# Performance work log

Measured on AMD Instinct MI355X. Metric: run time of the kernel, lower is better.

## Reference

```python
import jax, jax.numpy as jnp
import numpy as np

NH = 16   # num heads
CS = 16   # inner chunk size

def _gelu(x):
    return jax.nn.gelu(x, approximate=True)

def _diff_gelu(x):
    t = jnp.tanh(0.79788456 * x * (1.0 + 0.044715 * x * x))
    return 0.5 * x * ((1.0 - t * t) * (0.79788456 + 0.1070322243 * x * x)) + 0.5 * (1.0 + t)

def _ln_fused_l2_bwd(x, tgt, gamma, beta, eps=1e-6):
    # x, tgt: [B*nh, CS, f]; gamma/beta: [1, nh, 1, f]
    Bnh, N, HF = x.shape
    mu = x.mean(-1, keepdims=True)
    var = x.var(-1, keepdims=True)
    std = jnp.sqrt(var + eps)
    x_hat = (x - mu) / std
    y = gamma * x_hat.reshape(-1, NH, N, HF) + beta
    go = y - tgt.reshape(-1, NH, N, HF)
    gxh = (go * gamma).reshape(Bnh, N, HF)
    return (HF * gxh - gxh.sum(-1, keepdims=True) - x_hat * (gxh * x_hat).sum(-1, keepdims=True)) / (HF * std)

def setup_inputs() -> dict:
    key = jax.random.key(0)
    ks = jax.random.split(key, 8)
    B, nh, f, hf4, n_chunks = 4, NH, 64, 256, 128
    Bnh = B * nh
    XQ = jax.random.normal(ks[0], (n_chunks, Bnh, CS, f), jnp.float32)
    XK = jax.random.normal(ks[1], (n_chunks, Bnh, CS, f), jnp.float32)
    XV = jax.random.normal(ks[2], (n_chunks, Bnh, CS, f), jnp.float32)
    # inner-loop lr coeffs (ilr * token_idx ~ lr/head_dim): small positive
    coeff = jax.random.uniform(ks[3], (n_chunks, Bnh, CS, 1), jnp.float32) * 0.01
    coeff_last = jax.random.uniform(ks[4], (n_chunks, Bnh, 1, 1), jnp.float32) * 0.01
    W1 = jax.random.normal(ks[5], (Bnh, f, hf4), jnp.float32) * 0.02
    b1 = jnp.zeros((Bnh, 1, hf4), jnp.float32)
    W2 = jax.random.normal(ks[6], (Bnh, hf4, f), jnp.float32) * 0.02
    b2 = jnp.zeros((Bnh, 1, f), jnp.float32)
    ln_weight = jnp.ones((1, nh, 1, f), jnp.float32)
    ln_bias = jnp.zeros((1, nh, 1, f), jnp.float32)
    return dict(XQ=XQ, XK=XK, XV=XV, coeff=coeff, coeff_last=coeff_last,
                W1=W1, b1=b1, W2=W2, b2=b2, ln_weight=ln_weight, ln_bias=ln_bias)

def reference(XQ, XK, XV, coeff, coeff_last, W1, b1, W2, b2, ln_weight, ln_bias):
    n_chunks, Bnh, _, f = XQ.shape
    attn_b = jnp.tril(jnp.ones((CS, CS), XQ.dtype))

    def step(carry, inp):
        W1c, b1c, W2c, b2c = carry
        xv, xk, xq, c, cl = inp
        Z1 = xk @ W1c + b1c                      # [Bnh, CS, 4f]
        X2 = _gelu(Z1)
        Z2 = X2 @ W2c + b2c                      # [Bnh, CS, f]
        dZ2 = _ln_fused_l2_bwd(Z2, xv - xk, ln_weight, ln_bias)
        dZ1 = (dZ2 @ W2c.transpose(0, 2, 1)) * _diff_gelu(Z1)
        b1_bar = b1c - c * (attn_b @ dZ1)
        A1 = jnp.tril(xq @ xk.transpose(0, 2, 1))
        Z1_bar = xq @ W1c - c * (A1 @ dZ1) + b1_bar
        X2_bar = _gelu(Z1_bar)
        b2_bar = b2c - c * (attn_b @ dZ2)
        A2 = jnp.tril(X2_bar @ X2.transpose(0, 2, 1))
        Z2_bar = X2_bar @ W2c - c * (A2 @ dZ2) + b2_bar
        W1n = W1c - cl * (xk.transpose(0, 2, 1) @ dZ1)
        W2n = W2c - cl * (X2.transpose(0, 2, 1) @ dZ2)
        return (W1n, b1_bar[:, -1:], W2n, b2_bar[:, -1:]), Z2_bar

    _, Z2_all = jax.lax.scan(step, (W1, b1, W2, b2), (XV, XK, XQ, coeff, coeff_last))
    # [n_chunks, Bnh, CS, f] -> [Bnh, N, f]
    return Z2_all.transpose(1, 0, 2, 3).reshape(Bnh, n_chunks * CS, f)
```

## Files before the change

kernel.cpp:

```cpp
#include <hip/hip_runtime.h>

typedef __attribute__((ext_vector_type(8))) short bf16x8;
typedef __attribute__((ext_vector_type(4))) float f32x4;
typedef __attribute__((ext_vector_type(2))) unsigned int u32x2;

#define MFMA16(a,b,c) __builtin_amdgcn_mfma_f32_16x16x32_bf16(a,b,c,0,0,0)
#define A_GELU 0.7978845608028654f

#define OFF_W1B   0u
#define OFF_W2F   36864u
#define OFF_XK    70656u
#define OFF_XQ    72960u
#define OFF_X2    75264u
#define OFF_X2B   83712u
#define OFF_DZ2B  92160u
#define OFF_DZ1CT 94464u
#define OFF_DZ2CT 114944u
#define OFF_XKCT  120064u
#define OFF_X2CT  125184u
#define OFF_M1    145664u
#define OFF_M2    146944u
#define OFF_Z2F   148224u
#define OFF_Z2G   152576u
#define OFF_TGT   156928u
#define OFF_B2    161024u
#define OFF_COEF  161536u
#define OFF_CL    161600u
#define SMEM_BYTES 161616u

#define W2COL(col, row) ((col) ^ (((row)&7)<<3))

__device__ __forceinline__ float fast_tanh(float u){
    float e = __expf(2.0f*u);
    return 1.0f - 2.0f/(e + 1.0f);
}
__device__ __forceinline__ float gelu_f(float x){
    float t = fast_tanh(A_GELU*(x + 0.044715f*x*x*x));
    return 0.5f*x*(1.0f+t);
}
__device__ __forceinline__ float dgelu_f(float x){
    float x2 = x*x;
    float t = fast_tanh(A_GELU*x*(1.0f + 0.044715f*x2));
    return 0.5f*x*((1.0f-t*t)*(A_GELU + 0.1070322243f*x2)) + 0.5f*(1.0f+t);
}
__device__ __forceinline__ short f2bf(float f){
    unsigned u = __builtin_bit_cast(unsigned, f);
    u += 0x7FFFu + ((u >> 16) & 1u);
    return (short)(u >> 16);
}
__device__ __forceinline__ float bf2f(unsigned short s){
    unsigned u = ((unsigned)s) << 16;
    return __builtin_bit_cast(float, u);
}
__device__ __forceinline__ unsigned pkbf(float a, float b){
    unsigned r;
    asm("v_cvt_pk_bf16_f32 %0, %1, %2" : "=v"(r) : "v"(a), "v"(b));
    return r;
}
__device__ __forceinline__ bf16x8 ldfrag(const unsigned short* p){
    return *(const bf16x8*)p;
}

__global__ __launch_bounds__(512, 1)
void ttt_m2(const float* __restrict__ XQ, const float* __restrict__ XK,
            const float* __restrict__ XV, const float* __restrict__ coeff,
            const float* __restrict__ coeff_last,
            const float* __restrict__ W1g, const float* __restrict__ b1g,
            const float* __restrict__ W2g, const float* __restrict__ b2g,
            const float* __restrict__ gammag, const float* __restrict__ betag,
            float* __restrict__ out)
{
    const int h  = blockIdx.x;
    const int t  = threadIdx.x;
    const int l  = t & 63;
    const int w  = t >> 6;
    const int lo = l & 15;
    const int hi = l >> 4;

    extern __shared__ char smem[];
    unsigned short* sW1bu  = (unsigned short*)(smem + OFF_W1B);
    unsigned short* sW2fu  = (unsigned short*)(smem + OFF_W2F);
    unsigned short* sxku   = (unsigned short*)(smem + OFF_XK);
    unsigned short* sxqu   = (unsigned short*)(smem + OFF_XQ);
    unsigned short* sX2u   = (unsigned short*)(smem + OFF_X2);
    unsigned short* sX2bu  = (unsigned short*)(smem + OFF_X2B);
    unsigned short* sdZ2bu = (unsigned short*)(smem + OFF_DZ2B);
    unsigned short* sdZ1ct = (unsigned short*)(smem + OFF_DZ1CT);
    unsigned short* sdZ2ct = (unsigned short*)(smem + OFF_DZ2CT);
    unsigned short* sxkct  = (unsigned short*)(smem + OFF_XKCT);
    unsigned short* sX2ct  = (unsigned short*)(smem + OFF_X2CT);
    unsigned short* sM1u   = (unsigned short*)(smem + OFF_M1);
    unsigned short* sM2u   = (unsigned short*)(smem + OFF_M2);
    float* sZ2f  = (float*)(smem + OFF_Z2F);
    float* sZ2g  = (float*)(smem + OFF_Z2G);
    float* stgt  = (float*)(smem + OFF_TGT);
    float* b2f   = (float*)(smem + OFF_B2);
    float* scoef = (float*)(smem + OFF_COEF);
    float* sCL   = (float*)(smem + OFF_CL);

    const int base1 = h*16384;
    const int base2 = h*16384;

    float mW1[4][2][4];
    float mW2[2][4][4];
    #pragma unroll
    for (int mt = 0; mt < 4; ++mt)
      #pragma unroll
      for (int tix = 0; tix < 2; ++tix)
        #pragma unroll
        for (int reg = 0; reg < 4; ++reg) {
            const int m = mt*16 + hi*4 + reg, n = (2*w + tix)*16 + lo;
            mW1[mt][tix][reg] = W1g[base1 + m*256 + n];
        }
    #pragma unroll
    for (int mi = 0; mi < 2; ++mi)
      #pragma unroll
      for (int nt = 0; nt < 4; ++nt)
        #pragma unroll
        for (int reg = 0; reg < 4; ++reg) {
            const int m = (2*w + mi)*16 + hi*4 + reg, n = nt*16 + lo;
            mW2[mi][nt][reg] = W2g[base2 + m*64 + n];
        }
    float b1reg[2];
    b1reg[0] = b1g[h*256 + (2*w)*16 + lo];
    b1reg[1] = b1g[h*256 + (2*w+1)*16 + lo];

    for (int i = 0; i < 32; ++i) {
        const int idx = i*512 + t;
        const int m = idx >> 8, n = idx & 255;
        sW1bu[n*72 + m] = f2bf(W1g[base1 + idx]);
    }
    for (int i = 0; i < 32; ++i) {
        const int idx = i*512 + t;
        const int hf = idx >> 6, f = idx & 63;
        sW2fu[f*264 + W2COL(hf, f)] = f2bf(W2g[base2 + idx]);
    }
    if (t < 64) b2f[t] = b2g[h*64 + t];
    if (t < 256) {
        for (int k = 16; k < 40; ++k) { sdZ1ct[t*40 + k] = 0; sX2ct[t*40 + k] = 0; }
    }
    if (t < 64) {
        for (int k = 16; k < 40; ++k) { sdZ2ct[t*40 + k] = 0; sxkct[t*40 + k] = 0; }
    }
    if (t < 16) {
        for (int k = 16; k < 40; ++k) { sM1u[t*40 + k] = 0; sM2u[t*40 + k] = 0; }
    }

    const float gj = gammag[(h & 15)*64 + l];
    const float bj = betag [(h & 15)*64 + l];
    __syncthreads();

    for (int ci = 0; ci < 128; ++ci) {
        const int cb = ci*65536 + h*1024;

        {
            const int r0 = w*2;
            const float xk0 = XK[cb + r0*64 + l],     xq0 = XQ[cb + r0*64 + l];
            const float xk1 = XK[cb + (r0+1)*64 + l], xq1 = XQ[cb + (r0+1)*64 + l];
            const float xv0 = XV[cb + r0*64 + l],     xv1 = XV[cb + (r0+1)*64 + l];
            const unsigned pkk = pkbf(xk0, xk1);
            const unsigned pkq = pkbf(xq0, xq1);
            sxku[r0*72 + l]     = (unsigned short)pkk;
            sxku[(r0+1)*72 + l] = (unsigned short)(pkk >> 16);
            sxqu[r0*72 + l]     = (unsigned short)pkq;
            sxqu[(r0+1)*72 + l] = (unsigned short)(pkq >> 16);
            *(unsigned*)&sxkct[l*40 + r0] = pkk;
            stgt[r0*64 + l]     = xv0 - xk0;
            stgt[(r0+1)*64 + l] = xv1 - xk1;
        }
        if (t < 16)  scoef[t] = coeff[ci*1024 + h*16 + t];
        if (t == 16) sCL[0]   = coeff_last[ci*64 + h];
        __syncthreads();
        const float clv = sCL[0];
        const float c15 = scoef[15];

        float z1s[8];
        bf16x8 afk0 = ldfrag(sxku + lo*72 + hi*8);
        bf16x8 afk1 = ldfrag(sxku + lo*72 + 32 + hi*8);
        #pragma unroll
        for (int tix = 0; tix < 2; ++tix) {
            const int n = (2*w + tix)*16 + lo;
            f32x4 acc = {b1reg[tix], b1reg[tix], b1reg[tix], b1reg[tix]};
            acc = MFMA16(afk0, ldfrag(sW1bu + n*72 + hi*8), acc);
            acc = MFMA16(afk1, ldfrag(sW1bu + n*72 + 32 + hi*8), acc);
            float g[4];
            #pragma unroll
            for (int reg = 0; reg < 4; ++reg) {
                z1s[tix*4 + reg] = acc[reg];
                g[reg] = gelu_f(acc[reg]);
            }
            const unsigned p01 = pkbf(g[0], g[1]), p23 = pkbf(g[2], g[3]);
            sX2u[(hi*4+0)*264 + n] = (unsigned short)p01;
            sX2u[(hi*4+1)*264 + n] = (unsigned short)(p01 >> 16);
            sX2u[(hi*4+2)*264 + n] = (unsigned short)p23;
            sX2u[(hi*4+3)*264 + n] = (unsigned short)(p23 >> 16);
            *(u32x2*)&sX2ct[n*40 + hi*4] = (u32x2){p01, p23};
        }
        if (w == 0) {
            bf16x8 aq0 = ldfrag(sxqu + lo*72 + hi*8);
            bf16x8 aq1 = ldfrag(sxqu + lo*72 + 32 + hi*8);
            f32x4 a1 = {0.f, 0.f, 0.f, 0.f};
            a1 = MFMA16(aq0, afk0, a1);
            a1 = MFMA16(aq1, afk1, a1);
            #pragma unroll
            for (int reg = 0; reg < 4; ++reg) {
                const int r = hi*4 + reg;
                const float cr = scoef[r];
                const float v = (lo <= r) ? (-cr*(a1[reg] + 1.0f)) : 0.0f;
                sM1u[r*40 + lo] = f2bf(v);
            }
        }
        __syncthreads();

        const int tile = w & 3, kh = w >> 2;
        const int nf = tile*16 + lo;
        {
            f32x4 accPB;
            if (kh == 0) {
                const float b2v = b2f[(ci & 1)*64 + nf];
                accPB = (f32x4){b2v, b2v, b2v, b2v};
            } else accPB = (f32x4){0.f, 0.f, 0.f, 0.f};
            #pragma unroll
            for (int s = 0; s < 4; ++s) {
                const int k = (kh*4 + s)*32 + hi*8;
                accPB = MFMA16(ldfrag(sX2u + lo*264 + k),
                               ldfrag(sW2fu + nf*264 + W2COL(k, nf)), accPB);
            }
            float* dst = (kh == 0) ? sZ2g : sZ2f;
            #pragma unroll
            for (int reg = 0; reg < 4; ++reg)
                dst[(hi*4 + reg)*68 + nf] = accPB[reg];
        }
        __syncthreads();

        {
            float dzp[2];
            #pragma unroll
            for (int i = 0; i < 2; ++i) {
                const int r = w*2 + i;
                const float z2 = sZ2f[r*68 + l] + sZ2g[r*68 + l];
                float s1 = z2, s2 = z2*z2;
                #pragma unroll
                for (int m = 1; m < 64; m <<= 1) { s1 += __shfl_xor(s1, m); s2 += __shfl_xor(s2, m); }
                const float mu   = s1*(1.0f/64.0f);
                const float var  = s2*(1.0f/64.0f) - mu*mu;
                const float rstd = rsqrtf(var + 1e-6f);
                const float xh   = (z2 - mu)*rstd;
                const float go   = gj*xh + bj - stgt[r*64 + l];
                const float gg   = go*gj;
                float u1 = gg, u2 = gg*xh;
                #pragma unroll
                for (int m = 1; m < 64; m <<= 1) { u1 += __shfl_xor(u1, m); u2 += __shfl_xor(u2, m); }
                dzp[i] = (64.0f*gg - u1 - xh*u2)*(rstd*(1.0f/64.0f));
            }
            const unsigned pk = pkbf(dzp[0], dzp[1]);
            sdZ2bu[(w*2)*72 + l]   = (unsigned short)pk;
            sdZ2bu[(w*2+1)*72 + l] = (unsigned short)(pk >> 16);
            *(unsigned*)&sdZ2ct[l*40 + w*2] = pk;
        }
        __syncthreads();

        float b1old[2];
        {
            bf16x8 ad0 = ldfrag(sdZ2bu + lo*72 + hi*8);
            bf16x8 ad1 = ldfrag(sdZ2bu + lo*72 + 32 + hi*8);
            #pragma unroll
            for (int tix = 0; tix < 2; ++tix) {
                const int n = (2*w + tix)*16 + lo;
                f32x4 acc = {0.f, 0.f, 0.f, 0.f};
                bf16x8 bw;
                #pragma unroll
                for (int j = 0; j < 8; ++j)
                    bw[j] = (short)sW2fu[(hi*8 + j)*264 + (n ^ (j<<3))];
                acc = MFMA16(ad0, bw, acc);
                #pragma unroll
                for (int j = 0; j < 8; ++j)
                    bw[j] = (short)sW2fu[(32 + hi*8 + j)*264 + (n ^ (j<<3))];
                acc = MFMA16(ad1, bw, acc);
                float dv[4];
                float cs = 0.f;
                #pragma unroll
                for (int reg = 0; reg < 4; ++reg) {
                    dv[reg] = acc[reg]*dgelu_f(z1s[tix*4 + reg]);
                    cs += dv[reg];
                }
                *(u32x2*)&sdZ1ct[n*40 + hi*4] =
                    (u32x2){pkbf(dv[0], dv[1]), pkbf(dv[2], dv[3])};
                cs += __shfl_xor(cs, 16);
                cs += __shfl_xor(cs, 32);
                b1old[tix] = b1reg[tix];
                b1reg[tix] -= c15*cs;
            }
        }
        __syncthreads();

        {
            bf16x8 aq0 = ldfrag(sxqu + lo*72 + hi*8);
            bf16x8 aq1 = ldfrag(sxqu + lo*72 + 32 + hi*8);
            bf16x8 am1 = ldfrag(sM1u + lo*40 + hi*8);
            #pragma unroll
            for (int tix = 0; tix < 2; ++tix) {
                const int n = (2*w + tix)*16 + lo;
                f32x4 acc = {b1old[tix], b1old[tix], b1old[tix], b1old[tix]};
                acc = MFMA16(aq0, ldfrag(sW1bu + n*72 + hi*8), acc);
                acc = MFMA16(aq1, ldfrag(sW1bu + n*72 + 32 + hi*8), acc);
                acc = MFMA16(am1, ldfrag(sdZ1ct + n*40 + hi*8), acc);
                float g[4];
                #pragma unroll
                for (int reg = 0; reg < 4; ++reg) g[reg] = gelu_f(acc[reg]);
                const unsigned p01 = pkbf(g[0], g[1]), p23 = pkbf(g[2], g[3]);
                sX2bu[(hi*4+0)*264 + n] = (unsigned short)p01;
                sX2bu[(hi*4+1)*264 + n] = (unsigned short)(p01 >> 16);
                sX2bu[(hi*4+2)*264 + n] = (unsigned short)p23;
                sX2bu[(hi*4+3)*264 + n] = (unsigned short)(p23 >> 16);
            }
            bf16x8 bz0 = ldfrag(sdZ1ct + ((2*w)*16 + lo)*40 + hi*8);
            bf16x8 bz1 = ldfrag(sdZ1ct + ((2*w+1)*16 + lo)*40 + hi*8);
            #pragma unroll
            for (int mt = 0; mt < 4; ++mt) {
                bf16x8 axt = ldfrag(sxkct + (mt*16 + lo)*40 + hi*8);
                f32x4 z4 = {0.f,0.f,0.f,0.f};
                f32x4 u0 = MFMA16(axt, bz0, z4);
                f32x4 u1 = MFMA16(axt, bz1, z4);
                #pragma unroll
                for (int reg = 0; reg < 4; ++reg) {
                    mW1[mt][0][reg] -= clv*u0[reg];
                    mW1[mt][1][reg] -= clv*u1[reg];
                }
            }
        }
        __syncthreads();

        {
            bf16x8 bz2[4];
            #pragma unroll
            for (int nt = 0; nt < 4; ++nt)
                bz2[nt] = ldfrag(sdZ2ct + (nt*16 + lo)*40 + hi*8);
            #pragma unroll
            for (int mi = 0; mi < 2; ++mi) {
                bf16x8 ax2 = ldfrag(sX2ct + ((2*w + mi)*16 + lo)*40 + hi*8);
                #pragma unroll
                for (int nt = 0; nt < 4; ++nt) {
                    f32x4 z4 = {0.f,0.f,0.f,0.f};
                    f32x4 u = MFMA16(ax2, bz2[nt], z4);
                    #pragma unroll
                    for (int reg = 0; reg < 4; ++reg)
                        mW2[mi][nt][reg] -= clv*u[reg];
                }
            }
            if (w == 0) {
                f32x4 a2 = {0.f,0.f,0.f,0.f};
                #pragma unroll
                for (int ks = 0; ks < 8; ++ks) {
                    const int k = ks*32 + hi*8;
                    a2 = MFMA16(ldfrag(sX2bu + lo*264 + k),
                                ldfrag(sX2u + lo*264 + k), a2);
                }
                #pragma unroll
                for (int reg = 0; reg < 4; ++reg) {
                    const int r = hi*4 + reg;
                    const float cr = scoef[r];
                    const float v = (lo <= r) ? (-cr*(a2[reg] + 1.0f)) : 0.0f;
                    sM2u[r*40 + lo] = f2bf(v);
                }
            }
            if (w == 1) {
                float cs = 0.f;
                #pragma unroll
                for (int k = 0; k < 16; ++k) cs += bf2f(sdZ2ct[l*40 + k]);
                b2f[((ci+1) & 1)*64 + l] = b2f[(ci & 1)*64 + l] - c15*cs;
            }
        }
        __syncthreads();

        f32x4 accPF;
        if (kh == 0) {
            const float b2v = b2f[(ci & 1)*64 + nf];
            accPF = (f32x4){b2v, b2v, b2v, b2v};
        } else accPF = (f32x4){0.f, 0.f, 0.f, 0.f};
        #pragma unroll
        for (int s = 0; s < 4; ++s) {
            const int k = (kh*4 + s)*32 + hi*8;
            accPF = MFMA16(ldfrag(sX2bu + lo*264 + k),
                           ldfrag(sW2fu + nf*264 + W2COL(k, nf)), accPF);
        }
        if (kh == 0) {
            accPF = MFMA16(ldfrag(sM2u + lo*40 + hi*8),
                           ldfrag(sdZ2ct + nf*40 + hi*8), accPF);
        } else {
            #pragma unroll
            for (int reg = 0; reg < 4; ++reg)
                sZ2f[(hi*4 + reg)*68 + nf] = accPF[reg];
        }
        __syncthreads();

        if (kh == 0) {
            #pragma unroll
            for (int reg = 0; reg < 4; ++reg) {
                const int r = hi*4 + reg;
                out[h*131072 + (ci*16 + r)*64 + nf] = accPF[reg] + sZ2f[r*68 + nf];
            }
        }
        #pragma unroll
        for (int mt = 0; mt < 4; ++mt)
          #pragma unroll
          for (int tix = 0; tix < 2; ++tix) {
                const int n = (2*w + tix)*16 + lo, m0 = mt*16 + hi*4;
                *(u32x2*)&sW1bu[n*72 + m0] =
                    (u32x2){pkbf(mW1[mt][tix][0], mW1[mt][tix][1]),
                            pkbf(mW1[mt][tix][2], mW1[mt][tix][3])};
          }
        #pragma unroll
        for (int mi = 0; mi < 2; ++mi)
          #pragma unroll
          for (int nt = 0; nt < 4; ++nt) {
                const int n = nt*16 + lo, m0 = (2*w + mi)*16 + hi*4;
                *(u32x2*)&sW2fu[n*264 + (m0 ^ ((n&7)<<3))] =
                    (u32x2){pkbf(mW2[mi][nt][0], mW2[mi][nt][1]),
                            pkbf(mW2[mi][nt][2], mW2[mi][nt][3])};
          }
        __syncthreads();
    }
}

extern "C" void kernel_launch(void* const* d_in, const int* in_sizes, int n_in,
                              void* d_out, int out_size, void* d_ws, size_t ws_size,
                              hipStream_t stream) {
    const float* XQ  = (const float*)d_in[0];
    const float* XK  = (const float*)d_in[1];
    const float* XV  = (const float*)d_in[2];
    const float* cf  = (const float*)d_in[3];
    const float* cfl = (const float*)d_in[4];
    const float* W1  = (const float*)d_in[5];
    const float* b1  = (const float*)d_in[6];
    const float* W2  = (const float*)d_in[7];
    const float* b2  = (const float*)d_in[8];
    const float* gam = (const float*)d_in[9];
    const float* bet = (const float*)d_in[10];
    float* o = (float*)d_out;

    hipFuncSetAttribute((const void*)ttt_m2,
                        hipFuncAttributeMaxDynamicSharedMemorySize, SMEM_BYTES);
    ttt_m2<<<64, 512, SMEM_BYTES, stream>>>(XQ, XK, XV, cf, cfl, W1, b1, W2, b2, gam, bet, o);
}
```

Measured before the change: 1.070 ms.

## Double block to 1024 threads, double-buffer W2, prefetch next chunk inputs

Launches 16 waves per head instead of 8, so each wave owns one 16-column slice of the hidden dimension and one row of the layer-norm backward. W2 in shared memory is double-buffered, which lets the weight write-back merge into the preceding phase and drops a barrier and the split-K reduction for Z2. The next chunk's XK/XQ/XV and coefficients are prefetched into registers during the current chunk. Shared layouts get new XOR swizzles and narrower transposed buffers with masked fragment loads. The risks are more barrier participants per sync, idle waves during the w<4 phases, and higher shared-memory use.

```diff
diff --git a/kernel.cpp b/kernel.cpp
--- a/kernel.cpp
+++ b/kernel.cpp
@@ -8,27 +8,27 @@
 #define A_GELU 0.7978845608028654f
 
 #define OFF_W1B   0u
-#define OFF_W2F   36864u
-#define OFF_XK    70656u
-#define OFF_XQ    72960u
-#define OFF_X2    75264u
-#define OFF_X2B   83712u
-#define OFF_DZ2B  92160u
-#define OFF_DZ1CT 94464u
-#define OFF_DZ2CT 114944u
-#define OFF_XKCT  120064u
-#define OFF_X2CT  125184u
-#define OFF_M1    145664u
-#define OFF_M2    146944u
-#define OFF_Z2F   148224u
-#define OFF_Z2G   152576u
-#define OFF_TGT   156928u
-#define OFF_B2    161024u
-#define OFF_COEF  161536u
-#define OFF_CL    161600u
-#define SMEM_BYTES 161616u
-
-#define W2COL(col, row) ((col) ^ (((row)&7)<<3))
+#define OFF_W2F   32768u
+#define OFF_XK    98304u
+#define OFF_XQ    100608u
+#define OFF_X2    102912u
+#define OFF_X2B   111360u
+#define OFF_DZ2B  119808u
+#define OFF_DZ1CT 122112u
+#define OFF_DZ2CT 134400u
+#define OFF_XKCT  137472u
+#define OFF_X2CT  140544u
+#define OFF_M1    152832u
+#define OFF_M2    153600u
+#define OFF_Z2P   154368u
+#define OFF_TGT   158720u
+#define OFF_B2    162816u
+#define OFF_COEF  163328u
+#define OFF_CL    163392u
+#define SMEM_BYTES 163408u
+
+#define IDX_W1(n,m)  ((n)*64  + ((m)  ^ (((n)&7)<<3)))
+#define IDX_W2(f,hf) ((f)*256 + ((hf) ^ ((((f)>>3)&3)<<4)))
 
 __device__ __forceinline__ float fast_tanh(float u){
     float e = __expf(2.0f*u);
@@ -60,8 +60,13 @@
 __device__ __forceinline__ bf16x8 ldfrag(const unsigned short* p){
     return *(const bf16x8*)p;
 }
-
-__global__ __launch_bounds__(512, 1)
+__device__ __forceinline__ bf16x8 ldmask16(const unsigned short* row, int hi){
+    bf16x8 r = {0,0,0,0,0,0,0,0};
+    if (hi < 2) r = *(const bf16x8*)(row + hi*8);
+    return r;
+}
+
+__global__ __launch_bounds__(1024, 4)
 void ttt_m2(const float* __restrict__ XQ, const float* __restrict__ XK,
             const float* __restrict__ XV, const float* __restrict__ coeff,
             const float* __restrict__ coeff_last,
@@ -91,8 +96,7 @@
     unsigned short* sX2ct  = (unsigned short*)(smem + OFF_X2CT);
     unsigned short* sM1u   = (unsigned short*)(smem + OFF_M1);
     unsigned short* sM2u   = (unsigned short*)(smem + OFF_M2);
-    float* sZ2f  = (float*)(smem + OFF_Z2F);
-    float* sZ2g  = (float*)(smem + OFF_Z2G);
+    float* sZ2p  = (float*)(smem + OFF_Z2P);
     float* stgt  = (float*)(smem + OFF_TGT);
     float* b2f   = (float*)(smem + OFF_B2);
     float* scoef = (float*)(smem + OFF_COEF);
@@ -100,101 +104,95 @@
 
     const int base1 = h*16384;
     const int base2 = h*16384;
-
-    float mW1[4][2][4];
-    float mW2[2][4][4];
+    const int ncol  = w*16 + lo;
+    const int w1m   = (ncol & 7) << 3;
+    const int nfm   = ((ncol >> 3) & 3) << 4;
+
+    float mW1[4][4];
+    float mW2[4][4];
     #pragma unroll
     for (int mt = 0; mt < 4; ++mt)
       #pragma unroll
-      for (int tix = 0; tix < 2; ++tix)
-        #pragma unroll
-        for (int reg = 0; reg < 4; ++reg) {
-            const int m = mt*16 + hi*4 + reg, n = (2*w + tix)*16 + lo;
-            mW1[mt][tix][reg] = W1g[base1 + m*256 + n];
-        }
+      for (int reg = 0; reg < 4; ++reg)
+        mW1[mt][reg] = W1g[base1 + (mt*16 + hi*4 + reg)*256 + ncol];
     #pragma unroll
-    for (int mi = 0; mi < 2; ++mi)
+    for (int nt = 0; nt < 4; ++nt)
       #pragma unroll
-      for (int nt = 0; nt < 4; ++nt)
-        #pragma unroll
-        for (int reg = 0; reg < 4; ++reg) {
-            const int m = (2*w + mi)*16 + hi*4 + reg, n = nt*16 + lo;
-            mW2[mi][nt][reg] = W2g[base2 + m*64 + n];
-        }
-    float b1reg[2];
-    b1reg[0] = b1g[h*256 + (2*w)*16 + lo];
-    b1reg[1] = b1g[h*256 + (2*w+1)*16 + lo];
-
-    for (int i = 0; i < 32; ++i) {
-        const int idx = i*512 + t;
+      for (int reg = 0; reg < 4; ++reg)
+        mW2[nt][reg] = W2g[base2 + (w*16 + hi*4 + reg)*64 + nt*16 + lo];
+    float b1reg = b1g[h*256 + ncol];
+
+    #pragma unroll 4
+    for (int i = 0; i < 16; ++i) {
+        const int idx = i*1024 + t;
         const int m = idx >> 8, n = idx & 255;
-        sW1bu[n*72 + m] = f2bf(W1g[base1 + idx]);
+        sW1bu[IDX_W1(n, m)] = f2bf(W1g[base1 + idx]);
     }
-    for (int i = 0; i < 32; ++i) {
-        const int idx = i*512 + t;
+    #pragma unroll 4
+    for (int i = 0; i < 16; ++i) {
+        const int idx = i*1024 + t;
         const int hf = idx >> 6, f = idx & 63;
-        sW2fu[f*264 + W2COL(hf, f)] = f2bf(W2g[base2 + idx]);
+        sW2fu[IDX_W2(f, hf)] = f2bf(W2g[base2 + idx]);
     }
     if (t < 64) b2f[t] = b2g[h*64 + t];
-    if (t < 256) {
-        for (int k = 16; k < 40; ++k) { sdZ1ct[t*40 + k] = 0; sX2ct[t*40 + k] = 0; }
-    }
-    if (t < 64) {
-        for (int k = 16; k < 40; ++k) { sdZ2ct[t*40 + k] = 0; sxkct[t*40 + k] = 0; }
-    }
-    if (t < 16) {
-        for (int k = 16; k < 40; ++k) { sM1u[t*40 + k] = 0; sM2u[t*40 + k] = 0; }
-    }
 
     const float gj = gammag[(h & 15)*64 + l];
     const float bj = betag [(h & 15)*64 + l];
+
+    float pxk = XK[h*1024 + w*64 + l];
+    float pxq = XQ[h*1024 + w*64 + l];
+    float pxv = XV[h*1024 + w*64 + l];
+    float pcf = (t < 16)  ? coeff[h*16 + t] : 0.0f;
+    float pcl = (t == 16) ? coeff_last[h]   : 0.0f;
     __syncthreads();
 
     for (int ci = 0; ci < 128; ++ci) {
-        const int cb = ci*65536 + h*1024;
-
-        {
-            const int r0 = w*2;
-            const float xk0 = XK[cb + r0*64 + l],     xq0 = XQ[cb + r0*64 + l];
-            const float xk1 = XK[cb + (r0+1)*64 + l], xq1 = XQ[cb + (r0+1)*64 + l];
-            const float xv0 = XV[cb + r0*64 + l],     xv1 = XV[cb + (r0+1)*64 + l];
-            const unsigned pkk = pkbf(xk0, xk1);
-            const unsigned pkq = pkbf(xq0, xq1);
-            sxku[r0*72 + l]     = (unsigned short)pkk;
-            sxku[(r0+1)*72 + l] = (unsigned short)(pkk >> 16);
-            sxqu[r0*72 + l]     = (unsigned short)pkq;
-            sxqu[(r0+1)*72 + l] = (unsigned short)(pkq >> 16);
-            *(unsigned*)&sxkct[l*40 + r0] = pkk;
-            stgt[r0*64 + l]     = xv0 - xk0;
-            stgt[(r0+1)*64 + l] = xv1 - xk1;
-        }
-        if (t < 16)  scoef[t] = coeff[ci*1024 + h*16 + t];
-        if (t == 16) sCL[0]   = coeff_last[ci*64 + h];
+        const unsigned short* sW2p = sW2fu + (ci & 1)*16384;
+        unsigned short*       sW2q = sW2fu + ((ci & 1) ^ 1)*16384;
+
+        {
+            const unsigned short kk = (unsigned short)f2bf(pxk);
+            sxku[w*72 + l]  = kk;
+            sxkct[l*24 + w] = kk;
+            sxqu[w*72 + l]  = (unsigned short)f2bf(pxq);
+            stgt[w*64 + l]  = pxv - pxk;
+            if (t < 16)  scoef[t] = pcf;
+            if (t == 16) sCL[0]   = pcl;
+        }
         __syncthreads();
         const float clv = sCL[0];
         const float c15 = scoef[15];
-
-        float z1s[8];
+        float crs[4];
+        #pragma unroll
+        for (int reg = 0; reg < 4; ++reg) crs[reg] = scoef[hi*4 + reg];
+        if (ci < 127) {
+            const int cb1 = (ci + 1)*65536 + h*1024;
+            pxk = XK[cb1 + w*64 + l];
+            pxq = XQ[cb1 + w*64 + l];
+            pxv = XV[cb1 + w*64 + l];
+            if (t < 16)  pcf = coeff[(ci + 1)*1024 + h*16 + t];
+            if (t == 16) pcl = coeff_last[(ci + 1)*64 + h];
+        }
+
+        float z1s[4];
         bf16x8 afk0 = ldfrag(sxku + lo*72 + hi*8);
         bf16x8 afk1 = ldfrag(sxku + lo*72 + 32 + hi*8);
-        #pragma unroll
-        for (int tix = 0; tix < 2; ++tix) {
-            const int n = (2*w + tix)*16 + lo;
-            f32x4 acc = {b1reg[tix], b1reg[tix], b1reg[tix], b1reg[tix]};
-            acc = MFMA16(afk0, ldfrag(sW1bu + n*72 + hi*8), acc);
-            acc = MFMA16(afk1, ldfrag(sW1bu + n*72 + 32 + hi*8), acc);
+        {
+            f32x4 acc = {b1reg, b1reg, b1reg, b1reg};
+            acc = MFMA16(afk0, ldfrag(sW1bu + ncol*64 + ((hi*8)      ^ w1m)), acc);
+            acc = MFMA16(afk1, ldfrag(sW1bu + ncol*64 + ((32 + hi*8) ^ w1m)), acc);
             float g[4];
             #pragma unroll
             for (int reg = 0; reg < 4; ++reg) {
-                z1s[tix*4 + reg] = acc[reg];
+                z1s[reg] = acc[reg];
                 g[reg] = gelu_f(acc[reg]);
             }
             const unsigned p01 = pkbf(g[0], g[1]), p23 = pkbf(g[2], g[3]);
-            sX2u[(hi*4+0)*264 + n] = (unsigned short)p01;
-            sX2u[(hi*4+1)*264 + n] = (unsigned short)(p01 >> 16);
-            sX2u[(hi*4+2)*264 + n] = (unsigned short)p23;
-            sX2u[(hi*4+3)*264 + n] = (unsigned short)(p23 >> 16);
-            *(u32x2*)&sX2ct[n*40 + hi*4] = (u32x2){p01, p23};
+            sX2u[(hi*4+0)*264 + ncol] = (unsigned short)p01;
+            sX2u[(hi*4+1)*264 + ncol] = (unsigned short)(p01 >> 16);
+            sX2u[(hi*4+2)*264 + ncol] = (unsigned short)p23;
+            sX2u[(hi*4+3)*264 + ncol] = (unsigned short)(p23 >> 16);
+            *(u32x2*)&sX2ct[ncol*24 + hi*4] = (u32x2){p01, p23};
         }
         if (w == 0) {
             bf16x8 aq0 = ldfrag(sxqu + lo*72 + hi*8);
@@ -205,221 +203,168 @@
             #pragma unroll
             for (int reg = 0; reg < 4; ++reg) {
                 const int r = hi*4 + reg;
-                const float cr = scoef[r];
-                const float v = (lo <= r) ? (-cr*(a1[reg] + 1.0f)) : 0.0f;
-                sM1u[r*40 + lo] = f2bf(v);
-            }
-        }
-        __syncthreads();
-
-        const int tile = w & 3, kh = w >> 2;
-        const int nf = tile*16 + lo;
-        {
-            f32x4 accPB;
-            if (kh == 0) {
-                const float b2v = b2f[(ci & 1)*64 + nf];
-                accPB = (f32x4){b2v, b2v, b2v, b2v};
-            } else accPB = (f32x4){0.f, 0.f, 0.f, 0.f};
-            #pragma unroll
-            for (int s = 0; s < 4; ++s) {
-                const int k = (kh*4 + s)*32 + hi*8;
-                accPB = MFMA16(ldfrag(sX2u + lo*264 + k),
-                               ldfrag(sW2fu + nf*264 + W2COL(k, nf)), accPB);
-            }
-            float* dst = (kh == 0) ? sZ2g : sZ2f;
+                const float v = (lo <= r) ? (-crs[reg]*(a1[reg] + 1.0f)) : 0.0f;
+                sM1u[r*24 + lo] = f2bf(v);
+            }
+        }
+        __syncthreads();
+
+        if (w < 4) {
+            const float b2v = b2f[(ci & 1)*64 + ncol];
+            f32x4 acc = {b2v, b2v, b2v, b2v};
+            #pragma unroll
+            for (int s = 0; s < 8; ++s) {
+                const int k0 = s*32 + hi*8;
+                acc = MFMA16(ldfrag(sX2u + lo*264 + k0),
+                             ldfrag(sW2p + ncol*256 + (k0 ^ nfm)), acc);
+            }
             #pragma unroll
             for (int reg = 0; reg < 4; ++reg)
-                dst[(hi*4 + reg)*68 + nf] = accPB[reg];
-        }
-        __syncthreads();
-
-        {
-            float dzp[2];
-            #pragma unroll
-            for (int i = 0; i < 2; ++i) {
-                const int r = w*2 + i;
-                const float z2 = sZ2f[r*68 + l] + sZ2g[r*68 + l];
-                float s1 = z2, s2 = z2*z2;
-                #pragma unroll
-                for (int m = 1; m < 64; m <<= 1) { s1 += __shfl_xor(s1, m); s2 += __shfl_xor(s2, m); }
-                const float mu   = s1*(1.0f/64.0f);
-                const float var  = s2*(1.0f/64.0f) - mu*mu;
-                const float rstd = rsqrtf(var + 1e-6f);
-                const float xh   = (z2 - mu)*rstd;
-                const float go   = gj*xh + bj - stgt[r*64 + l];
-                const float gg   = go*gj;
-                float u1 = gg, u2 = gg*xh;
-                #pragma unroll
-                for (int m = 1; m < 64; m <<= 1) { u1 += __shfl_xor(u1, m); u2 += __shfl_xor(u2, m); }
-                dzp[i] = (64.0f*gg - u1 - xh*u2)*(rstd*(1.0f/64.0f));
-            }
-            const unsigned pk = pkbf(dzp[0], dzp[1]);
-            sdZ2bu[(w*2)*72 + l]   = (unsigned short)pk;
-            sdZ2bu[(w*2+1)*72 + l] = (unsigned short)(pk >> 16);
-            *(unsigned*)&sdZ2ct[l*40 + w*2] = pk;
-        }
-        __syncthreads();
-
-        float b1old[2];
+                sZ2p[(hi*4 + reg)*68 + ncol] = acc[reg];
+        }
+        __syncthreads();
+
+        {
+            const float z2 = sZ2p[w*68 + l];
+            float s1 = z2, s2 = z2*z2;
+            #pragma unroll
+            for (int m = 1; m < 64; m <<= 1) { s1 += __shfl_xor(s1, m); s2 += __shfl_xor(s2, m); }
+            const float mu   = s1*(1.0f/64.0f);
+            const float var  = s2*(1.0f/64.0f) - mu*mu;
+            const float rstd = rsqrtf(var + 1e-6f);
+            const float xh   = (z2 - mu)*rstd;
+            const float go   = gj*xh + bj - stgt[w*64 + l];
+            const float gg   = go*gj;
+            float u1 = gg, u2 = gg*xh;
+            #pragma unroll
+            for (int m = 1; m < 64; m <<= 1) { u1 += __shfl_xor(u1, m); u2 += __shfl_xor(u2, m); }
+            const float dz = (64.0f*gg - u1 - xh*u2)*(rstd*(1.0f/64.0f));
+            const unsigned short hv = (unsigned short)f2bf(dz);
+            sdZ2bu[w*72 + l]  = hv;
+            sdZ2ct[l*24 + w]  = hv;
+        }
+        __syncthreads();
+
+        float b1old;
         {
             bf16x8 ad0 = ldfrag(sdZ2bu + lo*72 + hi*8);
             bf16x8 ad1 = ldfrag(sdZ2bu + lo*72 + 32 + hi*8);
-            #pragma unroll
-            for (int tix = 0; tix < 2; ++tix) {
-                const int n = (2*w + tix)*16 + lo;
-                f32x4 acc = {0.f, 0.f, 0.f, 0.f};
-                bf16x8 bw;
-                #pragma unroll
-                for (int j = 0; j < 8; ++j)
-                    bw[j] = (short)sW2fu[(hi*8 + j)*264 + (n ^ (j<<3))];
-                acc = MFMA16(ad0, bw, acc);
-                #pragma unroll
-                for (int j = 0; j < 8; ++j)
-                    bw[j] = (short)sW2fu[(32 + hi*8 + j)*264 + (n ^ (j<<3))];
-                acc = MFMA16(ad1, bw, acc);
-                float dv[4];
-                float cs = 0.f;
-                #pragma unroll
-                for (int reg = 0; reg < 4; ++reg) {
-                    dv[reg] = acc[reg]*dgelu_f(z1s[tix*4 + reg]);
-                    cs += dv[reg];
-                }
-                *(u32x2*)&sdZ1ct[n*40 + hi*4] =
-                    (u32x2){pkbf(dv[0], dv[1]), pkbf(dv[2], dv[3])};
-                cs += __shfl_xor(cs, 16);
-                cs += __shfl_xor(cs, 32);
-                b1old[tix] = b1reg[tix];
-                b1reg[tix] -= c15*cs;
-            }
+            const int colA = ncol ^ ((hi & 3) << 4);
+            bf16x8 bw0, bw1;
+            #pragma unroll
+            for (int j = 0; j < 8; ++j) {
+                bw0[j] = (short)sW2p[(hi*8 + j)*256 + colA];
+                bw1[j] = (short)sW2p[(32 + hi*8 + j)*256 + colA];
+            }
+            f32x4 acc = {0.f, 0.f, 0.f, 0.f};
+            acc = MFMA16(ad0, bw0, acc);
+            acc = MFMA16(ad1, bw1, acc);
+            float dv[4], cs = 0.f;
+            #pragma unroll
+            for (int reg = 0; reg < 4; ++reg) {
+                dv[reg] = acc[reg]*dgelu_f(z1s[reg]);
+                cs += dv[reg];
+            }
+            *(u32x2*)&sdZ1ct[ncol*24 + hi*4] =
+                (u32x2){pkbf(dv[0], dv[1]), pkbf(dv[2], dv[3])};
+            cs += __shfl_xor(cs, 16);
+            cs += __shfl_xor(cs, 32);
+            b1old = b1reg;
+            b1reg -= c15*cs;
         }
         __syncthreads();
 
         {
             bf16x8 aq0 = ldfrag(sxqu + lo*72 + hi*8);
             bf16x8 aq1 = ldfrag(sxqu + lo*72 + 32 + hi*8);
-            bf16x8 am1 = ldfrag(sM1u + lo*40 + hi*8);
-            #pragma unroll
-            for (int tix = 0; tix < 2; ++tix) {
-                const int n = (2*w + tix)*16 + lo;
-                f32x4 acc = {b1old[tix], b1old[tix], b1old[tix], b1old[tix]};
-                acc = MFMA16(aq0, ldfrag(sW1bu + n*72 + hi*8), acc);
-                acc = MFMA16(aq1, ldfrag(sW1bu + n*72 + 32 + hi*8), acc);
-                acc = MFMA16(am1, ldfrag(sdZ1ct + n*40 + hi*8), acc);
-                float g[4];
-                #pragma unroll
-                for (int reg = 0; reg < 4; ++reg) g[reg] = gelu_f(acc[reg]);
-                const unsigned p01 = pkbf(g[0], g[1]), p23 = pkbf(g[2], g[3]);
-                sX2bu[(hi*4+0)*264 + n] = (unsigned short)p01;
-                sX2bu[(hi*4+1)*264 + n] = (unsigned short)(p01 >> 16);
-                sX2bu[(hi*4+2)*264 + n] = (unsigned short)p23;
-                sX2bu[(hi*4+3)*264 + n] = (unsigned short)(p23 >> 16);
-            }
-            bf16x8 bz0 = ldfrag(sdZ1ct + ((2*w)*16 + lo)*40 + hi*8);
-            bf16x8 bz1 = ldfrag(sdZ1ct + ((2*w+1)*16 + lo)*40 + hi*8);
+            bf16x8 bdz1 = ldmask16(sdZ1ct + ncol*24, hi);
+            f32x4 acc = {b1old, b1old, b1old, b1old};
+            acc = MFMA16(aq0, ldfrag(sW1bu + ncol*64 + ((hi*8)      ^ w1m)), acc);
+            acc = MFMA16(aq1, ldfrag(sW1bu + ncol*64 + ((32 + hi*8) ^ w1m)), acc);
+            acc = MFMA16(ldmask16(sM1u + lo*24, hi), bdz1, acc);
+            float g[4];
+            #pragma unroll
+            for (int reg = 0; reg < 4; ++reg) g[reg] = gelu_f(acc[reg]);
+            const unsigned p01 = pkbf(g[0], g[1]), p23 = pkbf(g[2], g[3]);
+            sX2bu[(hi*4+0)*264 + ncol] = (unsigned short)p01;
+            sX2bu[(hi*4+1)*264 + ncol] = (unsigned short)(p01 >> 16);
+            sX2bu[(hi*4+2)*264 + ncol] = (unsigned short)p23;
+            sX2bu[(hi*4+3)*264 + ncol] = (unsigned short)(p23 >> 16);
             #pragma unroll
             for (int mt = 0; mt < 4; ++mt) {
-                bf16x8 axt = ldfrag(sxkct + (mt*16 + lo)*40 + hi*8);
-                f32x4 z4 = {0.f,0.f,0.f,0.f};
-                f32x4 u0 = MFMA16(axt, bz0, z4);
-                f32x4 u1 = MFMA16(axt, bz1, z4);
-                #pragma unroll
-                for (int reg = 0; reg < 4; ++reg) {
-                    mW1[mt][0][reg] -= clv*u0[reg];
-                    mW1[mt][1][reg] -= clv*u1[reg];
-                }
-            }
-        }
-        __syncthreads();
-
-        {
-            bf16x8 bz2[4];
-            #pragma unroll
-            for (int nt = 0; nt < 4; ++nt)
-                bz2[nt] = ldfrag(sdZ2ct + (nt*16 + lo)*40 + hi*8);
-            #pragma unroll
-            for (int mi = 0; mi < 2; ++mi) {
-                bf16x8 ax2 = ldfrag(sX2ct + ((2*w + mi)*16 + lo)*40 + hi*8);
-                #pragma unroll
-                for (int nt = 0; nt < 4; ++nt) {
-                    f32x4 z4 = {0.f,0.f,0.f,0.f};
-                    f32x4 u = MFMA16(ax2, bz2[nt], z4);
-                    #pragma unroll
-                    for (int reg = 0; reg < 4; ++reg)
-                        mW2[mi][nt][reg] -= clv*u[reg];
-                }
+                bf16x8 axt = ldmask16(sxkct + (mt*16 + lo)*24, hi);
+                f32x4 z4 = {0.f, 0.f, 0.f, 0.f};
+                f32x4 u = MFMA16(axt, bdz1, z4);
+                #pragma unroll
+                for (int reg = 0; reg < 4; ++reg) mW1[mt][reg] -= clv*u[reg];
+            }
+        }
+        __syncthreads();
+
+        {
+            bf16x8 ax2 = ldmask16(sX2ct + ncol*24, hi);
+            #pragma unroll
+            for (int nt = 0; nt < 4; ++nt) {
+                bf16x8 bz2 = ldmask16(sdZ2ct + (nt*16 + lo)*24, hi);
+                f32x4 z4 = {0.f, 0.f, 0.f, 0.f};
+                f32x4 u = MFMA16(ax2, bz2, z4);
+                #pragma unroll
+                for (int reg = 0; reg < 4; ++reg) mW2[nt][reg] -= clv*u[reg];
             }
             if (w == 0) {
-                f32x4 a2 = {0.f,0.f,0.f,0.f};
-                #pragma unroll
-                for (int ks = 0; ks < 8; ++ks) {
-                    const int k = ks*32 + hi*8;
-                    a2 = MFMA16(ldfrag(sX2bu + lo*264 + k),
-                                ldfrag(sX2u + lo*264 + k), a2);
+                f32x4 a2 = {0.f, 0.f, 0.f, 0.f};
+                #pragma unroll
+                for (int s = 0; s < 8; ++s) {
+                    const int k0 = s*32 + hi*8;
+                    a2 = MFMA16(ldfrag(sX2bu + lo*264 + k0),
+                                ldfrag(sX2u + lo*264 + k0), a2);
                 }
                 #pragma unroll
                 for (int reg = 0; reg < 4; ++reg) {
                     const int r = hi*4 + reg;
-                    const float cr = scoef[r];
-                    const float v = (lo <= r) ? (-cr*(a2[reg] + 1.0f)) : 0.0f;
-                    sM2u[r*40 + lo] = f2bf(v);
+                    const float v = (lo <= r) ? (-crs[reg]*(a2[reg] + 1.0f)) : 0.0f;
+                    sM2u[r*24 + lo] = f2bf(v);
                 }
             }
             if (w == 1) {
                 float cs = 0.f;
                 #pragma unroll
-                for (int k = 0; k < 16; ++k) cs += bf2f(sdZ2ct[l*40 + k]);
-                b2f[((ci+1) & 1)*64 + l] = b2f[(ci & 1)*64 + l] - c15*cs;
-            }
-        }
-        __syncthreads();
-
-        f32x4 accPF;
-        if (kh == 0) {
-            const float b2v = b2f[(ci & 1)*64 + nf];
-            accPF = (f32x4){b2v, b2v, b2v, b2v};
-        } else accPF = (f32x4){0.f, 0.f, 0.f, 0.f};
-        #pragma unroll
-        for (int s = 0; s < 4; ++s) {
-            const int k = (kh*4 + s)*32 + hi*8;
-            accPF = MFMA16(ldfrag(sX2bu + lo*264 + k),
-                           ldfrag(sW2fu + nf*264 + W2COL(k, nf)), accPF);
-        }
-        if (kh == 0) {
-            accPF = MFMA16(ldfrag(sM2u + lo*40 + hi*8),
-                           ldfrag(sdZ2ct + nf*40 + hi*8), accPF);
-        } else {
+                for (int k = 0; k < 16; ++k) cs += bf2f(sdZ2bu[k*72 + l]);
+                b2f[((ci + 1) & 1)*64 + l] = b2f[(ci & 1)*64 + l] - c15*cs;
+            }
+            #pragma unroll
+            for (int mt = 0; mt < 4; ++mt) {
+                const int m0 = mt*16 + hi*4;
+                *(u32x2*)&sW1bu[ncol*64 + (m0 ^ w1m)] =
+                    (u32x2){pkbf(mW1[mt][0], mW1[mt][1]),
+                            pkbf(mW1[mt][2], mW1[mt][3])};
+            }
+            const int m0 = w*16 + hi*4;
+            #pragma unroll
+            for (int nt = 0; nt < 4; ++nt) {
+                const int f = nt*16 + lo;
+                *(u32x2*)&sW2q[f*256 + (m0 ^ (((f >> 3) & 3) << 4))] =
+                    (u32x2){pkbf(mW2[nt][0], mW2[nt][1]),
+                            pkbf(mW2[nt][2], mW2[nt][3])};
+            }
+        }
+        __syncthreads();
+
+        if (w < 4) {
+            const float b2v = b2f[(ci & 1)*64 + ncol];
+            f32x4 acc = {b2v, b2v, b2v, b2v};
+            #pragma unroll
+            for (int s = 0; s < 8; ++s) {
+                const int k0 = s*32 + hi*8;
+                acc = MFMA16(ldfrag(sX2bu + lo*264 + k0),
+                             ldfrag(sW2p + ncol*256 + (k0 ^ nfm)), acc);
+            }
+            acc = MFMA16(ldmask16(sM2u + lo*24, hi),
+                         ldmask16(sdZ2ct + ncol*24, hi), acc);
             #pragma unroll
             for (int reg = 0; reg < 4; ++reg)
-                sZ2f[(hi*4 + reg)*68 + nf] = accPF[reg];
-        }
-        __syncthreads();
-
-        if (kh == 0) {
-            #pragma unroll
-            for (int reg = 0; reg < 4; ++reg) {
-                const int r = hi*4 + reg;
-                out[h*131072 + (ci*16 + r)*64 + nf] = accPF[reg] + sZ2f[r*68 + nf];
-            }
-        }
-        #pragma unroll
-        for (int mt = 0; mt < 4; ++mt)
-          #pragma unroll
-          for (int tix = 0; tix < 2; ++tix) {
-                const int n = (2*w + tix)*16 + lo, m0 = mt*16 + hi*4;
-                *(u32x2*)&sW1bu[n*72 + m0] =
-                    (u32x2){pkbf(mW1[mt][tix][0], mW1[mt][tix][1]),
-                            pkbf(mW1[mt][tix][2], mW1[mt][tix][3])};
-          }
-        #pragma unroll
-        for (int mi = 0; mi < 2; ++mi)
-          #pragma unroll
-          for (int nt = 0; nt < 4; ++nt) {
-                const int n = nt*16 + lo, m0 = (2*w + mi)*16 + hi*4;
-                *(u32x2*)&sW2fu[n*264 + (m0 ^ ((n&7)<<3))] =
-                    (u32x2){pkbf(mW2[mi][nt][0], mW2[mi][nt][1]),
-                            pkbf(mW2[mi][nt][2], mW2[mi][nt][3])};
-          }
-        __syncthreads();
+                out[h*131072 + (ci*16 + hi*4 + reg)*64 + ncol] = acc[reg];
+        }
     }
 }
 
@@ -441,5 +386,5 @@
 
     hipFuncSetAttribute((const void*)ttt_m2,
                         hipFuncAttributeMaxDynamicSharedMemorySize, SMEM_BYTES);
-    ttt_m2<<<64, 512, SMEM_BYTES, stream>>>(XQ, XK, XV, cf, cfl, W1, b1, W2, b2, gam, bet, o);
-}
+    ttt_m2<<<64, 1024, SMEM_BYTES, stream>>>(XQ, XK, XV, cf, cfl, W1, b1, W2, b2, gam, bet, o);
+}
```

Result: slower. 1.525 ms (+42.5%).
